# Kernel optimization log

Measured on AMD Instinct MI355X. Metric: run time of the kernel, lower is better.

## Reference

```python
import jax, jax.numpy as jnp
import numpy as np

B, N, DIM = 1, 4096, 512
HEADS, LOCAL_HEADS = 8, 4           # int(8*0.6)=4 local, 4 content
CONTENT_HEADS = HEADS - LOCAL_HEADS
HEAD_DIM = DIM // HEADS             # 64
WINDOW = 64                         # == H == W so window attention is well-formed
TOPK_RATIO = 0.2
SCALE = HEAD_DIM ** -0.5


def _window_partition(x, ws):
    Bb, H, W, C = x.shape
    pad_h = (ws - H % ws) % ws
    pad_w = (ws - W % ws) % ws
    x = jnp.pad(x, ((0, 0), (0, pad_h), (0, pad_w), (0, 0)))
    Hp, Wp = H + pad_h, W + pad_w
    x = x.reshape(Bb, Hp // ws, ws, Wp // ws, ws, C)
    win = x.transpose(0, 1, 3, 2, 4, 5).reshape(-1, ws, ws, C)
    return win, (Hp, Wp)


def _window_unpartition(win, ws, pad_hw, hw):
    Hp, Wp = pad_hw
    H, W = hw
    Bb = win.shape[0] // (Hp * Wp // ws // ws)
    x = win.reshape(Bb, Hp // ws, Wp // ws, ws, ws, -1)
    x = x.transpose(0, 1, 3, 2, 4, 5).reshape(Bb, Hp, Wp, -1)
    return x[:, :H, :W, :]


def setup_inputs() -> dict:
    key = jax.random.key(0)
    ks = jax.random.split(key, 12)
    s = 0.02
    f32 = jnp.float32
    ld = LOCAL_HEADS * HEAD_DIM      # 256
    cd = CONTENT_HEADS * HEAD_DIM    # 256
    return {
        'x': jax.random.normal(ks[0], (B, N, DIM), f32),
        'W_lqkv': jax.random.normal(ks[1], (DIM, 3 * ld), f32) * s,
        'b_lqkv': jnp.zeros((3 * ld,), f32),
        'W_cqkv': jax.random.normal(ks[2], (DIM, 3 * cd), f32) * s,
        'b_cqkv': jnp.zeros((3 * cd,), f32),
        'W_lproj': jax.random.normal(ks[3], (ld, DIM), f32) * s,
        'b_lproj': jnp.zeros((DIM,), f32),
        'W_cproj': jax.random.normal(ks[4], (cd, DIM), f32) * s,
        'b_cproj': jnp.zeros((DIM,), f32),
        'W_s1': jax.random.normal(ks[5], (DIM, DIM // 2), f32) * s,
        'b_s1': jnp.zeros((DIM // 2,), f32),
        'W_s2': jax.random.normal(ks[6], (DIM // 2, 1), f32) * s,
        'b_s2': jnp.zeros((1,), f32),
    }


def reference(x, W_lqkv, b_lqkv, W_cqkv, b_cqkv, W_lproj, b_lproj,
              W_cproj, b_cproj, W_s1, b_s1, W_s2, b_s2):
    Bb, Nn, C = x.shape
    H = W = int(np.sqrt(Nn))

    # ---- local (windowed) attention branch ----
    x_sp = x.reshape(Bb, H, W, C)
    x_win, pad_hw = _window_partition(x_sp, WINDOW)           # (Bw, ws, ws, C)
    Bw, Hw, Ww, _ = x_win.shape
    Nw = Hw * Ww
    xl = x_win.reshape(Bw, Nw, C)
    lqkv = (xl @ W_lqkv + b_lqkv).reshape(Bw, Nw, 3, LOCAL_HEADS, HEAD_DIM)
    lqkv = lqkv.transpose(2, 0, 3, 1, 4)                      # (3, Bw, h, Nw, d)
    lq, lk, lv = lqkv[0], lqkv[1], lqkv[2]
    lattn = jnp.einsum('bhqd,bhkd->bhqk', lq, lk) * SCALE
    lattn = jax.nn.softmax(lattn, axis=-1)
    lo = jnp.einsum('bhqk,bhkd->bhqd', lattn, lv)
    lo = lo.transpose(0, 2, 1, 3).reshape(Bw, Hw, Ww, LOCAL_HEADS * HEAD_DIM)
    lo = _window_unpartition(lo, WINDOW, pad_hw, (H, W)).reshape(Bb, Nn, -1)
    local_x = lo @ W_lproj + b_lproj

    # ---- saliency-gated content-based sparse attention branch ----
    h = jax.nn.gelu(x @ W_s1 + b_s1, approximate=False)
    scores = (h @ W_s2 + b_s2)[..., 0]                        # (B, N)
    K = max(1, int(Nn * TOPK_RATIO))
    _, idx = jax.lax.top_k(scores, K)                         # (B, K)
    mask = jnp.zeros((Bb, Nn), bool).at[jnp.arange(Bb)[:, None], idx].set(True)

    cqkv = (x @ W_cqkv + b_cqkv).reshape(Bb, Nn, 3, CONTENT_HEADS, HEAD_DIM)
    cqkv = cqkv.transpose(2, 0, 3, 1, 4)
    cq, ck, cv = cqkv[0], cqkv[1], cqkv[2]
    cattn = jnp.einsum('bhqd,bhkd->bhqk', cq, ck) * SCALE
    cattn = jnp.where(mask[:, None, None, :], cattn, -jnp.inf)
    cattn = jax.nn.softmax(cattn, axis=-1)
    co = jnp.einsum('bhqk,bhkd->bhqd', cattn, cv)
    co = co.transpose(0, 2, 1, 3).reshape(Bb, Nn, CONTENT_HEADS * HEAD_DIM)
    content_x = co @ W_cproj + b_cproj

    out = local_x + content_x
    attn = jnp.concatenate([lattn.mean(axis=1), cattn.mean(axis=1)], axis=1)
    return out, attn
```

## Files before the change

### kernel.cpp

```cpp
#include <hip/hip_runtime.h>

typedef __bf16 bf16;
typedef __bf16 bf16x8 __attribute__((ext_vector_type(8)));
typedef float  floatx4 __attribute__((ext_vector_type(4)));

#define SCALE 0.125f

__device__ __forceinline__ floatx4 mfma16(bf16x8 a, bf16x8 b, floatx4 c) {
    return __builtin_amdgcn_mfma_f32_16x16x32_bf16(a, b, c, 0, 0, 0);
}

__device__ __forceinline__ bf16x8 load_f32_as_bf16x8(const float* p) {
    float4 f0 = *(const float4*)p;
    float4 f1 = *(const float4*)(p + 4);
    bf16x8 a;
    a[0] = (bf16)f0.x; a[1] = (bf16)f0.y; a[2] = (bf16)f0.z; a[3] = (bf16)f0.w;
    a[4] = (bf16)f1.x; a[5] = (bf16)f1.y; a[6] = (bf16)f1.z; a[7] = (bf16)f1.w;
    return a;
}

__global__ void k_transpose(const float* __restrict__ src, bf16* __restrict__ dst,
                            int R, int C) {
    __shared__ float tile[32][33];
    int c0 = blockIdx.x * 32, r0 = blockIdx.y * 32;
    int tx = threadIdx.x, ty = threadIdx.y;
    for (int i = ty; i < 32; i += 8) {
        int r = r0 + i, c = c0 + tx;
        tile[i][tx] = (r < R && c < C) ? src[r * C + c] : 0.f;
    }
    __syncthreads();
    for (int i = ty; i < 32; i += 8) {
        int r = r0 + tx, c = c0 + i;
        if (r < R && c < C) dst[(size_t)c * R + r] = (bf16)tile[tx][i];
    }
}

__global__ __launch_bounds__(256) void k_qkv(
    const float* __restrict__ x,
    const bf16* __restrict__ WlT, const bf16* __restrict__ WcT,
    const float* __restrict__ b_l, const float* __restrict__ b_c,
    bf16* __restrict__ lq, bf16* __restrict__ lk, bf16* __restrict__ lvT,
    bf16* __restrict__ cq, bf16* __restrict__ ck, bf16* __restrict__ cv)
{
    const int tid = threadIdx.x;
    const int wave = tid >> 6, lane = tid & 63;
    const int ln15 = lane & 15, quad = lane >> 4;
    const int m0 = blockIdx.x * 64 + wave * 16;
    const int n0 = blockIdx.y * 64;

    floatx4 acc[4];
    for (int s = 0; s < 4; ++s) acc[s] = (floatx4){0.f, 0.f, 0.f, 0.f};

    for (int k0 = 0; k0 < 512; k0 += 32) {
        bf16x8 a = load_f32_as_bf16x8(x + (m0 + ln15) * 512 + k0 + quad * 8);
        for (int s = 0; s < 4; ++s) {
            int cg = n0 + s * 16 + ln15;
            const bf16* bt = (cg < 768) ? (WlT + cg * 512) : (WcT + (cg - 768) * 512);
            bf16x8 b = *(const bf16x8*)(bt + k0 + quad * 8);
            acc[s] = mfma16(a, b, acc[s]);
        }
    }

    for (int s = 0; s < 4; ++s) {
        int cg = n0 + s * 16 + ln15;
        for (int r = 0; r < 4; ++r) {
            int row = m0 + quad * 4 + r;
            float v = acc[s][r];
            if (cg < 768) {
                v += b_l[cg];
                int qkv = cg >> 8, hh = (cg >> 6) & 3, d = cg & 63;
                bf16 bv = (bf16)v;
                if (qkv == 0)      lq[(hh * 4096 + row) * 64 + d] = bv;
                else if (qkv == 1) lk[(hh * 4096 + row) * 64 + d] = bv;
                else               lvT[(hh * 64 + d) * 4096 + row] = bv;
            } else {
                int c = cg - 768;
                v += b_c[c];
                int qkv = c >> 8, hh = (c >> 6) & 3, d = c & 63;
                bf16 bv = (bf16)v;
                if (qkv == 0)      cq[(hh * 4096 + row) * 64 + d] = bv;
                else if (qkv == 1) ck[(hh * 4096 + row) * 64 + d] = bv;
                else               cv[(hh * 4096 + row) * 64 + d] = bv;
            }
        }
    }
}

__global__ __launch_bounds__(256) void k_scores(
    const float* __restrict__ x, const float* __restrict__ Ws1,
    const float* __restrict__ bs1, const float* __restrict__ Ws2,
    const float* __restrict__ bs2, float* __restrict__ scores)
{
    __shared__ float xs[4][512];
    int row0 = blockIdx.x * 4;
    int t = threadIdx.x;
    for (int i = t; i < 512; i += 256) {
        int r = i >> 7, k4 = (i & 127) * 4;
        *(float4*)&xs[r][k4] = *(const float4*)&x[(row0 + r) * 512 + k4];
    }
    __syncthreads();
    int r = t >> 6, cb = (t & 63) * 4;
    float acc[4] = {0.f, 0.f, 0.f, 0.f};
    #pragma unroll 4
    for (int k = 0; k < 512; ++k) {
        float a = xs[r][k];
        float4 w = *(const float4*)(Ws1 + k * 256 + cb);
        acc[0] = fmaf(a, w.x, acc[0]); acc[1] = fmaf(a, w.y, acc[1]);
        acc[2] = fmaf(a, w.z, acc[2]); acc[3] = fmaf(a, w.w, acc[3]);
    }
    float s = 0.f;
    for (int j = 0; j < 4; ++j) {
        float v = acc[j] + bs1[cb + j];
        float g = 0.5f * v * (1.0f + erff(v * 0.70710678118654752f));
        s = fmaf(g, Ws2[cb + j], s);
    }
    s += __shfl_xor(s, 1, 64);  s += __shfl_xor(s, 2, 64);
    s += __shfl_xor(s, 4, 64);  s += __shfl_xor(s, 8, 64);
    s += __shfl_xor(s, 16, 64); s += __shfl_xor(s, 32, 64);
    if ((t & 63) == 0) scores[row0 + r] = s + bs2[0];
}

__global__ __launch_bounds__(1024) void k_topk(const float* __restrict__ scores,
                                               int* __restrict__ sel, int* __restrict__ pos) {
    __shared__ unsigned long long key[4096];
    int tid = threadIdx.x;
    for (int i = tid; i < 4096; i += 1024) {
        unsigned u = __float_as_uint(scores[i]);
        u = (u & 0x80000000u) ? ~u : (u | 0x80000000u);
        key[i] = ((unsigned long long)u << 32) | (unsigned)(~i);
        pos[i] = -1;
    }
    __syncthreads();
    for (int k = 2; k <= 4096; k <<= 1) {
        for (int j = k >> 1; j > 0; j >>= 1) {
            for (int i = tid; i < 4096; i += 1024) {
                int ixj = i ^ j;
                if (ixj > i) {
                    unsigned long long a = key[i], b = key[ixj];
                    bool desc = (i & k) == 0;
                    if (desc ? (a < b) : (a > b)) { key[i] = b; key[ixj] = a; }
                }
            }
            __syncthreads();
        }
    }
    for (int r = tid; r < 819; r += 1024) {
        int idx = (int)(~(unsigned)(key[r] & 0xFFFFFFFFu));
        sel[r] = idx;
        pos[idx] = r;
    }
}

__global__ __launch_bounds__(256) void k_gather(
    const bf16* __restrict__ ck, const bf16* __restrict__ cv,
    const int* __restrict__ sel,
    bf16* __restrict__ ckg, bf16* __restrict__ cvgT)
{
    int g = blockIdx.x * 4 + (threadIdx.x >> 6);
    int d = threadIdx.x & 63;
    int hh = g / 896, r = g % 896;
    int src = (r < 819) ? sel[r] : -1;
    bf16 kv = (src >= 0) ? ck[(hh * 4096 + src) * 64 + d] : (bf16)0.0f;
    bf16 vv = (src >= 0) ? cv[(hh * 4096 + src) * 64 + d] : (bf16)0.0f;
    ckg[(hh * 896 + r) * 64 + d] = kv;
    cvgT[(hh * 64 + d) * 896 + r] = vv;
}

__global__ __launch_bounds__(256, 5) void k_pass2b(
    const bf16* __restrict__ lq, const bf16* __restrict__ lk, const bf16* __restrict__ lvT,
    const bf16* __restrict__ cq, const bf16* __restrict__ ckg, const bf16* __restrict__ cvgT,
    float* __restrict__ partOL,
    float* __restrict__ partOC,
    float* __restrict__ partSL,
    float* __restrict__ partSC)
{
    __shared__ __align__(16) bf16 pbuf[4][2][16 * 40];
    int wave = threadIdx.x >> 6, lane = threadIdx.x & 63;
    int ln15 = lane & 15, quad = lane >> 4;
    int m0 = blockIdx.x * 64 + wave * 16;
    int y = blockIdx.y;
    bool local = y < 32;
    int h     = local ? (y >> 3) : ((y - 32) >> 1);
    int split = local ? (y & 7) : ((y - 32) & 1);
    int NV    = local ? 4096 : 896;
    int kbeg  = local ? split * 512 : split * 448;
    int kcnt  = local ? 512 : 448;

    const bf16* Qh = (local ? lq : cq) + (h * 4096 + m0) * 64;
    const bf16* Kh = (local ? lk : ckg) + h * NV * 64;
    const bf16* Vh = (local ? lvT : cvgT) + h * 64 * NV;

    bf16x8 af0 = *(const bf16x8*)(Qh + ln15 * 64 + quad * 8);
    bf16x8 af1 = *(const bf16x8*)(Qh + ln15 * 64 + 32 + quad * 8);

    floatx4 o[4];
    #pragma unroll
    for (int ds = 0; ds < 4; ++ds) o[ds] = (floatx4){0.f, 0.f, 0.f, 0.f};
    float se[4] = {0.f, 0.f, 0.f, 0.f};

    const int rdoff = (ln15 * 80 + quad * 16) ^ (((ln15 >> 3) & 1) << 4);

    for (int key0 = kbeg; key0 < kbeg + kcnt; key0 += 64) {
        #pragma unroll
        for (int c = 0; c < 2; ++c) {
            int kb = key0 + c * 32;
            char* pb = (char*)&pbuf[wave][c][0];
            #pragma unroll
            for (int s = 0; s < 2; ++s) {
                int kc = kb + s * 16;
                const bf16* krow = Kh + (kc + ln15) * 64;
                floatx4 z0 = (floatx4){0.f, 0.f, 0.f, 0.f};
                floatx4 z1 = (floatx4){0.f, 0.f, 0.f, 0.f};
                z0 = mfma16(af0, *(const bf16x8*)(krow + quad * 8), z0);
                z1 = mfma16(af1, *(const bf16x8*)(krow + 32 + quad * 8), z1);
                bool valid = local || (kc + ln15) < 819;
                #pragma unroll
                for (int r = 0; r < 4; ++r) {
                    float zz = z0[r] + z1[r];
                    float p = valid ? __expf(fminf(zz * SCALE, 60.f)) : 0.0f;
                    se[r] += p;
                    int row = quad * 4 + r;
                    int wo = (row * 80 + s * 32 + ln15 * 2) ^ (((row >> 3) & 1) << 4);
                    *(bf16*)(pb + wo) = (bf16)p;
                }
            }
        }
        #pragma unroll
        for (int c = 0; c < 2; ++c) {
            int kb = key0 + c * 32;
            bf16x8 ap = *(const bf16x8*)((const char*)&pbuf[wave][c][0] + rdoff);
            #pragma unroll
            for (int ds = 0; ds < 4; ++ds) {
                const bf16* vrow = Vh + (ds * 16 + ln15) * NV + kb + quad * 8;
                o[ds] = mfma16(ap, *(const bf16x8*)vrow, o[ds]);
            }
        }
    }

    float* ps = (local ? partSL : partSC) + (split * 4 + h) * 4096;
    #pragma unroll
    for (int r = 0; r < 4; ++r) {
        float s = se[r];
        s += __shfl_xor(s, 1, 64);
        s += __shfl_xor(s, 2, 64);
        s += __shfl_xor(s, 4, 64);
        s += __shfl_xor(s, 8, 64);
        if (ln15 == 0) ps[m0 + quad * 4 + r] = s;
    }

    float* ob = (local ? partOL : partOC) + (size_t)split * (4096 * 256);
    #pragma unroll
    for (int ds = 0; ds < 4; ++ds)
        for (int r = 0; r < 4; ++r)
            ob[(m0 + quad * 4 + r) * 256 + h * 64 + ds * 16 + ln15] = o[ds][r];
}

__global__ __launch_bounds__(256) void k_reduce2(
    const float* __restrict__ partOL, const float* __restrict__ partOC,
    const float* __restrict__ partSL, const float* __restrict__ partSC,
    float* __restrict__ lsum, float* __restrict__ lo, float* __restrict__ co)
{
    int t = threadIdx.x;
    int q0 = blockIdx.x * 4;
    int r = t >> 6, cc = (t & 63) * 4;
    int q = q0 + r;
    int h = cc >> 6;

    float sl = 0.f;
    #pragma unroll
    for (int s = 0; s < 8; ++s) sl += partSL[(s * 4 + h) * 4096 + q];
    float rll = 1.0f / fmaxf(sl, 1e-30f);
    float a0 = 0.f, a1 = 0.f, a2 = 0.f, a3 = 0.f;
    #pragma unroll
    for (int s = 0; s < 8; ++s) {
        float4 v = *(const float4*)(partOL + (size_t)s * 1048576 + q * 256 + cc);
        a0 += v.x; a1 += v.y; a2 += v.z; a3 += v.w;
    }
    *(float4*)(lo + q * 256 + cc) = (float4){a0 * rll, a1 * rll, a2 * rll, a3 * rll};

    float sc = partSC[h * 4096 + q] + partSC[(4 + h) * 4096 + q];
    float rlc = 1.0f / fmaxf(sc, 1e-30f);
    float4 v0 = *(const float4*)(partOC + q * 256 + cc);
    float4 v1 = *(const float4*)(partOC + 1048576 + q * 256 + cc);
    *(float4*)(co + q * 256 + cc) = (float4){(v0.x + v1.x) * rlc, (v0.y + v1.y) * rlc,
                                             (v0.z + v1.z) * rlc, (v0.w + v1.w) * rlc};

    if (t < 32) {
        int h8 = t >> 2, rr = t & 3, qq = q0 + rr;
        float s = 0.f;
        if (h8 < 4) {
            #pragma unroll
            for (int sp = 0; sp < 8; ++sp) s += partSL[(sp * 4 + h8) * 4096 + qq];
        } else {
            s = partSC[(h8 - 4) * 4096 + qq] + partSC[(4 + h8 - 4) * 4096 + qq];
        }
        lsum[h8 * 4096 + qq] = s;
    }
}

__global__ __launch_bounds__(256) void k_pass2a(
    const bf16* __restrict__ lq, const bf16* __restrict__ lk,
    const bf16* __restrict__ cq, const bf16* __restrict__ ckg,
    const float* __restrict__ lsum,
    float* __restrict__ attn_local,
    bf16* __restrict__ pcomp)
{
    int wave = threadIdx.x >> 6, lane = threadIdx.x & 63;
    int ln15 = lane & 15, quad = lane >> 4;
    int m0 = blockIdx.x * 64 + wave * 16;
    int y = blockIdx.y;
    bool local = y < 32;
    const bf16* Q  = local ? lq : cq;
    const bf16* Kt = local ? lk : ckg;
    int NV = local ? 4096 : 896;
    int kbeg = local ? y * 128 : (y - 32) * 128;
    int kend = kbeg + 128;
    int hbase = local ? 0 : 4;

    bf16x8 af[4][2];
    #pragma unroll
    for (int h2 = 0; h2 < 4; ++h2)
        for (int ks = 0; ks < 2; ++ks)
            af[h2][ks] = *(const bf16x8*)(Q + (h2 * 4096 + m0 + ln15) * 64 + ks * 32 + quad * 8);

    float rl[4][4];
    #pragma unroll
    for (int h2 = 0; h2 < 4; ++h2)
        for (int r = 0; r < 4; ++r)
            rl[h2][r] = 0.25f / fmaxf(lsum[(hbase + h2) * 4096 + m0 + quad * 4 + r], 1e-30f);

    for (int key0 = kbeg; key0 < kend; key0 += 32) {
        float pm[2][4] = {{0.f, 0.f, 0.f, 0.f}, {0.f, 0.f, 0.f, 0.f}};
        #pragma unroll
        for (int h2 = 0; h2 < 4; ++h2) {
            #pragma unroll
            for (int s = 0; s < 2; ++s) {
                int kc = key0 + s * 16;
                const bf16* krow = Kt + (h2 * NV + kc + ln15) * 64;
                floatx4 z = (floatx4){0.f, 0.f, 0.f, 0.f};
                z = mfma16(af[h2][0], *(const bf16x8*)(krow + quad * 8), z);
                z = mfma16(af[h2][1], *(const bf16x8*)(krow + 32 + quad * 8), z);
                bool valid = local || (kc + ln15) < 819;
                if (valid)
                    for (int r = 0; r < 4; ++r)
                        pm[s][r] += __expf(fminf(z[r] * SCALE, 60.f)) * rl[h2][r];
            }
        }
        if (local) {
            #pragma unroll
            for (int s = 0; s < 2; ++s)
                for (int r = 0; r < 4; ++r)
                    attn_local[(m0 + quad * 4 + r) * 4096 + key0 + s * 16 + ln15] = pm[s][r];
        } else {
            #pragma unroll
            for (int s = 0; s < 2; ++s) {
                int kc = key0 + s * 16 + ln15;
                if (kc < 832)
                    for (int r = 0; r < 4; ++r)
                        pcomp[(m0 + quad * 4 + r) * 832 + kc] = (bf16)(pm[s][r]);
            }
        }
    }
}

__global__ __launch_bounds__(256) void k_expand(const bf16* __restrict__ pcomp,
                                                const int* __restrict__ pos,
                                                float* __restrict__ attn_content) {
    int row = blockIdx.x;
    int c0 = threadIdx.x * 16;
    const bf16* prow = pcomp + row * 832;
    float vals[16];
    #pragma unroll
    for (int j = 0; j < 16; ++j) {
        int p = pos[c0 + j];
        vals[j] = (p >= 0) ? (float)prow[p] : 0.0f;
    }
    float* dst = attn_content + (size_t)row * 4096 + c0;
    *(float4*)(dst)      = (float4){vals[0], vals[1], vals[2], vals[3]};
    *(float4*)(dst + 4)  = (float4){vals[4], vals[5], vals[6], vals[7]};
    *(float4*)(dst + 8)  = (float4){vals[8], vals[9], vals[10], vals[11]};
    *(float4*)(dst + 12) = (float4){vals[12], vals[13], vals[14], vals[15]};
}

__global__ __launch_bounds__(256) void k_proj(
    const float* __restrict__ lo, const float* __restrict__ co,
    const bf16* __restrict__ WlpT, const bf16* __restrict__ WcpT,
    const float* __restrict__ bl, const float* __restrict__ bc,
    float* __restrict__ out)
{
    const int tid = threadIdx.x;
    const int wave = tid >> 6, lane = tid & 63;
    const int ln15 = lane & 15, quad = lane >> 4;
    const int m0 = blockIdx.x * 64 + wave * 16;
    const int n0 = blockIdx.y * 64;

    floatx4 acc[4];
    for (int s = 0; s < 4; ++s) acc[s] = (floatx4){0.f, 0.f, 0.f, 0.f};

    for (int k0 = 0; k0 < 256; k0 += 32) {
        bf16x8 al = load_f32_as_bf16x8(lo + (m0 + ln15) * 256 + k0 + quad * 8);
        bf16x8 ac = load_f32_as_bf16x8(co + (m0 + ln15) * 256 + k0 + quad * 8);
        for (int s = 0; s < 4; ++s) {
            int c = n0 + s * 16 + ln15;
            acc[s] = mfma16(al, *(const bf16x8*)(WlpT + c * 256 + k0 + quad * 8), acc[s]);
            acc[s] = mfma16(ac, *(const bf16x8*)(WcpT + c * 256 + k0 + quad * 8), acc[s]);
        }
    }
    for (int s = 0; s < 4; ++s) {
        int c = n0 + s * 16 + ln15;
        float bias = bl[c] + bc[c];
        for (int r = 0; r < 4; ++r)
            out[(m0 + quad * 4 + r) * 512 + c] = acc[s][r] + bias;
    }
}

#define OFF_WLQKVT  0L
#define OFF_WCQKVT  786432L
#define OFF_LQ      1572864L
#define OFF_LK      3670016L
#define OFF_LVT     5767168L
#define OFF_CQ      7864320L
#define OFF_CK      9961472L
#define OFF_CV      12058624L
#define OFF_PCOMP   9961472L
#define OFF_CKG     16777216L
#define OFF_CVGT    17235968L
#define OFF_WLPT    16777216L
#define OFF_WCPT    17039360L
#define OFF_SCORES  17694720L
#define OFF_SEL     17711104L
#define OFF_POS     17715200L
#define OFF_LSUM    17731584L
#define OFF_LO      17862656L
#define OFF_CO      22056960L
#define WS_TOTAL    26251264L

extern "C" void kernel_launch(void* const* d_in, const int* in_sizes, int n_in,
                              void* d_out, int out_size, void* d_ws, size_t ws_size,
                              hipStream_t stream) {
    if (ws_size < (size_t)WS_TOTAL) return;

    const float* x       = (const float*)d_in[0];
    const float* W_lqkv  = (const float*)d_in[1];
    const float* b_lqkv  = (const float*)d_in[2];
    const float* W_cqkv  = (const float*)d_in[3];
    const float* b_cqkv  = (const float*)d_in[4];
    const float* W_lproj = (const float*)d_in[5];
    const float* b_lproj = (const float*)d_in[6];
    const float* W_cproj = (const float*)d_in[7];
    const float* b_cproj = (const float*)d_in[8];
    const float* W_s1    = (const float*)d_in[9];
    const float* b_s1    = (const float*)d_in[10];
    const float* W_s2    = (const float*)d_in[11];
    const float* b_s2    = (const float*)d_in[12];

    char* ws = (char*)d_ws;
    bf16* WlqkvT  = (bf16*)(ws + OFF_WLQKVT);
    bf16* WcqkvT  = (bf16*)(ws + OFF_WCQKVT);
    bf16* lq    = (bf16*)(ws + OFF_LQ);
    bf16* lk    = (bf16*)(ws + OFF_LK);
    bf16* lvT   = (bf16*)(ws + OFF_LVT);
    bf16* cq    = (bf16*)(ws + OFF_CQ);
    bf16* ck    = (bf16*)(ws + OFF_CK);
    bf16* cv    = (bf16*)(ws + OFF_CV);
    bf16* pcomp = (bf16*)(ws + OFF_PCOMP);
    bf16* ckg   = (bf16*)(ws + OFF_CKG);
    bf16* cvgT  = (bf16*)(ws + OFF_CVGT);
    bf16* WlpT  = (bf16*)(ws + OFF_WLPT);
    bf16* WcpT  = (bf16*)(ws + OFF_WCPT);
    float* scores  = (float*)(ws + OFF_SCORES);
    int*   sel     = (int*)(ws + OFF_SEL);
    int*   pos     = (int*)(ws + OFF_POS);
    float* lsum    = (float*)(ws + OFF_LSUM);
    float* lo      = (float*)(ws + OFF_LO);
    float* co      = (float*)(ws + OFF_CO);

    float* outp = (float*)d_out;
    float* attn_local   = outp + 2097152;
    float* attn_content = attn_local + 4096 * 4096;
    float* partOL = attn_content;
    float* partOC = attn_content + 8388608;
    float* partSL = attn_content + 10485760;
    float* partSC = attn_content + 10616832;

    k_transpose<<<dim3(24, 16), dim3(32, 8), 0, stream>>>(W_lqkv, WlqkvT, 512, 768);
    k_transpose<<<dim3(24, 16), dim3(32, 8), 0, stream>>>(W_cqkv, WcqkvT, 512, 768);

    k_qkv<<<dim3(64, 24), 256, 0, stream>>>(x, WlqkvT, WcqkvT, b_lqkv, b_cqkv,
                                            lq, lk, lvT, cq, ck, cv);
    k_scores<<<1024, 256, 0, stream>>>(x, W_s1, b_s1, W_s2, b_s2, scores);
    k_topk<<<1, 1024, 0, stream>>>(scores, sel, pos);
    k_gather<<<896, 256, 0, stream>>>(ck, cv, sel, ckg, cvgT);
    k_pass2b<<<dim3(64, 40), 256, 0, stream>>>(lq, lk, lvT, cq, ckg, cvgT,
                                               partOL, partOC, partSL, partSC);
    k_reduce2<<<1024, 256, 0, stream>>>(partOL, partOC, partSL, partSC, lsum, lo, co);
    k_pass2a<<<dim3(64, 39), 256, 0, stream>>>(lq, lk, cq, ckg, lsum,
                                               attn_local, pcomp);
    k_transpose<<<dim3(16, 8), dim3(32, 8), 0, stream>>>(W_lproj, WlpT, 256, 512);
    k_transpose<<<dim3(16, 8), dim3(32, 8), 0, stream>>>(W_cproj, WcpT, 256, 512);
    k_expand<<<4096, 256, 0, stream>>>(pcomp, pos, attn_content);
    k_proj<<<dim3(64, 8), 256, 0, stream>>>(lo, co, WlpT, WcpT, b_lproj, b_cproj, outp);
}
```

Baseline: 697.9 us.

## Fold softmax scale into Q, replace bitonic top-k with radix select, simplify P buffer

Pre-scales Q by 0.125 when writing the QKV projection output, so the attention kernels no longer multiply every score by SCALE. It also replaces the full 4096-element bitonic sort in top-k with a histogram radix select plus a brute-force rank inside the boundary bin. Finally it fuses the two QK MFMAs into one accumulator chain and drops the XOR swizzle on the P scratch buffer in favour of padded indexing. The top-k change cuts many barrier-separated sort stages, but the boundary-bin rank is quadratic and the selection order now comes from atomics. Scaling Q before the bf16 cast also slightly changes rounding.

```diff
diff --git a/kernel.cpp b/kernel.cpp
--- a/kernel.cpp
+++ b/kernel.cpp
@@ -3,8 +3,6 @@
 typedef __bf16 bf16;
 typedef __bf16 bf16x8 __attribute__((ext_vector_type(8)));
 typedef float  floatx4 __attribute__((ext_vector_type(4)));
-
-#define SCALE 0.125f
 
 __device__ __forceinline__ floatx4 mfma16(bf16x8 a, bf16x8 b, floatx4 c) {
     return __builtin_amdgcn_mfma_f32_16x16x32_bf16(a, b, c, 0, 0, 0);
@@ -69,18 +67,16 @@
             if (cg < 768) {
                 v += b_l[cg];
                 int qkv = cg >> 8, hh = (cg >> 6) & 3, d = cg & 63;
-                bf16 bv = (bf16)v;
-                if (qkv == 0)      lq[(hh * 4096 + row) * 64 + d] = bv;
-                else if (qkv == 1) lk[(hh * 4096 + row) * 64 + d] = bv;
-                else               lvT[(hh * 64 + d) * 4096 + row] = bv;
+                if (qkv == 0)      lq[(hh * 4096 + row) * 64 + d] = (bf16)(v * 0.125f);
+                else if (qkv == 1) lk[(hh * 4096 + row) * 64 + d] = (bf16)v;
+                else               lvT[(hh * 64 + d) * 4096 + row] = (bf16)v;
             } else {
                 int c = cg - 768;
                 v += b_c[c];
                 int qkv = c >> 8, hh = (c >> 6) & 3, d = c & 63;
-                bf16 bv = (bf16)v;
-                if (qkv == 0)      cq[(hh * 4096 + row) * 64 + d] = bv;
-                else if (qkv == 1) ck[(hh * 4096 + row) * 64 + d] = bv;
-                else               cv[(hh * 4096 + row) * 64 + d] = bv;
+                if (qkv == 0)      cq[(hh * 4096 + row) * 64 + d] = (bf16)(v * 0.125f);
+                else if (qkv == 1) ck[(hh * 4096 + row) * 64 + d] = (bf16)v;
+                else               cv[(hh * 4096 + row) * 64 + d] = (bf16)v;
             }
         }
     }
@@ -122,32 +118,75 @@
 
 __global__ __launch_bounds__(1024) void k_topk(const float* __restrict__ scores,
                                                int* __restrict__ sel, int* __restrict__ pos) {
-    __shared__ unsigned long long key[4096];
+    __shared__ unsigned ubuf[4096];
+    __shared__ unsigned cga[2048], cgb[2048];
+    __shared__ int bidx[1024];
+    __shared__ int ctr, bctr, Bbin;
     int tid = threadIdx.x;
+    if (tid == 0) { ctr = 0; bctr = 0; }
+    for (int i = tid; i < 2048; i += 1024) cga[i] = 0u;
+    __syncthreads();
     for (int i = tid; i < 4096; i += 1024) {
-        unsigned u = __float_as_uint(scores[i]);
-        u = (u & 0x80000000u) ? ~u : (u | 0x80000000u);
-        key[i] = ((unsigned long long)u << 32) | (unsigned)(~i);
+        unsigned s = __float_as_uint(scores[i]);
+        unsigned u = (s & 0x80000000u) ? ~s : (s | 0x80000000u);
+        ubuf[i] = u;
         pos[i] = -1;
+        atomicAdd(&cga[u >> 21], 1u);
     }
     __syncthreads();
-    for (int k = 2; k <= 4096; k <<= 1) {
-        for (int j = k >> 1; j > 0; j >>= 1) {
-            for (int i = tid; i < 4096; i += 1024) {
-                int ixj = i ^ j;
-                if (ixj > i) {
-                    unsigned long long a = key[i], b = key[ixj];
-                    bool desc = (i & k) == 0;
-                    if (desc ? (a < b) : (a > b)) { key[i] = b; key[ixj] = a; }
-                }
-            }
-            __syncthreads();
-        }
-    }
-    for (int r = tid; r < 819; r += 1024) {
-        int idx = (int)(~(unsigned)(key[r] & 0xFFFFFFFFu));
-        sel[r] = idx;
-        pos[idx] = r;
+    unsigned* src = cga; unsigned* dst = cgb;
+    for (int off = 1; off < 2048; off <<= 1) {
+        for (int i = tid; i < 2048; i += 1024)
+            dst[i] = src[i] + ((i + off < 2048) ? src[i + off] : 0u);
+        __syncthreads();
+        unsigned* tmp = src; src = dst; dst = tmp;
+    }
+    for (int b = tid; b < 2048; b += 1024) {
+        unsigned ge = src[b];
+        unsigned gt = (b < 2047) ? src[b + 1] : 0u;
+        if (ge >= 819u && gt < 819u) Bbin = b;
+    }
+    __syncthreads();
+    int B = Bbin;
+    int countAbove = (B < 2047) ? (int)src[B + 1] : 0;
+    int need = 819 - countAbove;
+    for (int i = tid; i < 4096; i += 1024) {
+        int b = (int)(ubuf[i] >> 21);
+        if (b > B) {
+            int slot = atomicAdd(&ctr, 1);
+            sel[slot] = i;
+            pos[i] = slot;
+        } else if (b == B) {
+            int ls = atomicAdd(&bctr, 1);
+            if (ls < 1024) bidx[ls] = i;
+        }
+    }
+    __syncthreads();
+    int m = bctr;
+    if (m <= 1024) {
+        for (int e = tid; e < m; e += 1024) {
+            int i = bidx[e];
+            unsigned ui = ubuf[i];
+            int rank = 0;
+            for (int j = 0; j < m; ++j) {
+                int ij = bidx[j];
+                unsigned uj = ubuf[ij];
+                rank += (uj > ui || (uj == ui && ij < i)) ? 1 : 0;
+            }
+            if (rank < need) { int slot = countAbove + rank; sel[slot] = i; pos[i] = slot; }
+        }
+    } else {
+        for (int i = tid; i < 4096; i += 1024) {
+            if ((int)(ubuf[i] >> 21) != B) continue;
+            unsigned ui = ubuf[i];
+            int rank = 0;
+            for (int j = 0; j < 4096; ++j) {
+                if ((int)(ubuf[j] >> 21) != B) continue;
+                unsigned uj = ubuf[j];
+                rank += (uj > ui || (uj == ui && j < i)) ? 1 : 0;
+            }
+            if (rank < need) { int slot = countAbove + rank; sel[slot] = i; pos[i] = slot; }
+        }
     }
 }
 
@@ -198,37 +237,31 @@
     for (int ds = 0; ds < 4; ++ds) o[ds] = (floatx4){0.f, 0.f, 0.f, 0.f};
     float se[4] = {0.f, 0.f, 0.f, 0.f};
 
-    const int rdoff = (ln15 * 80 + quad * 16) ^ (((ln15 >> 3) & 1) << 4);
-
     for (int key0 = kbeg; key0 < kbeg + kcnt; key0 += 64) {
         #pragma unroll
         for (int c = 0; c < 2; ++c) {
             int kb = key0 + c * 32;
-            char* pb = (char*)&pbuf[wave][c][0];
+            bf16* pb = &pbuf[wave][c][0];
             #pragma unroll
             for (int s = 0; s < 2; ++s) {
                 int kc = kb + s * 16;
                 const bf16* krow = Kh + (kc + ln15) * 64;
-                floatx4 z0 = (floatx4){0.f, 0.f, 0.f, 0.f};
-                floatx4 z1 = (floatx4){0.f, 0.f, 0.f, 0.f};
-                z0 = mfma16(af0, *(const bf16x8*)(krow + quad * 8), z0);
-                z1 = mfma16(af1, *(const bf16x8*)(krow + 32 + quad * 8), z1);
+                floatx4 z = mfma16(af1, *(const bf16x8*)(krow + 32 + quad * 8),
+                            mfma16(af0, *(const bf16x8*)(krow + quad * 8),
+                                   (floatx4){0.f, 0.f, 0.f, 0.f}));
                 bool valid = local || (kc + ln15) < 819;
                 #pragma unroll
                 for (int r = 0; r < 4; ++r) {
-                    float zz = z0[r] + z1[r];
-                    float p = valid ? __expf(fminf(zz * SCALE, 60.f)) : 0.0f;
+                    float p = valid ? __expf(fminf(z[r], 60.f)) : 0.0f;
                     se[r] += p;
-                    int row = quad * 4 + r;
-                    int wo = (row * 80 + s * 32 + ln15 * 2) ^ (((row >> 3) & 1) << 4);
-                    *(bf16*)(pb + wo) = (bf16)p;
+                    pb[(quad * 4 + r) * 40 + s * 16 + ln15] = (bf16)p;
                 }
             }
         }
         #pragma unroll
         for (int c = 0; c < 2; ++c) {
             int kb = key0 + c * 32;
-            bf16x8 ap = *(const bf16x8*)((const char*)&pbuf[wave][c][0] + rdoff);
+            bf16x8 ap = *(const bf16x8*)(&pbuf[wave][c][0] + ln15 * 40 + quad * 8);
             #pragma unroll
             for (int ds = 0; ds < 4; ++ds) {
                 const bf16* vrow = Vh + (ds * 16 + ln15) * NV + kb + quad * 8;
@@ -343,7 +376,7 @@
                 bool valid = local || (kc + ln15) < 819;
                 if (valid)
                     for (int r = 0; r < 4; ++r)
-                        pm[s][r] += __expf(fminf(z[r] * SCALE, 60.f)) * rl[h2][r];
+                        pm[s][r] += __expf(fminf(z[r], 60.f)) * rl[h2][r];
             }
         }
         if (local) {
```

After: 660.4 us. 5.4% less time.
